# Kernel optimization log

Measured on AMD Instinct MI355X. Metric: run time of the kernel, lower is better.

Reference implementation:

```python
import jax, jax.numpy as jnp
import numpy as np

C = 256      # MSA_channels
PC = 256     # pair_channels
G = 4        # groups
GP = C // G  # group_planes
FF = 4 * C
EPS = 1e-5


def layernorm(x, w, b):
    mu = jnp.mean(x, axis=-1, keepdims=True)
    var = jnp.mean(jnp.square(x - mu), axis=-1, keepdims=True)
    return (x - mu) * jax.lax.rsqrt(var + EPS) * w + b


def setup_inputs() -> dict:
    key = jax.random.key(0)
    ks = jax.random.split(key, 12)
    N, D, L = 1, 64, 512
    s = lambda fan_in: 1.0 / np.sqrt(fan_in)
    return {
        "msa_matrix": jax.random.normal(ks[0], (N, D, L, C), jnp.float32),
        "rr_edge": jax.random.normal(ks[1], (N, L, L, PC), jnp.float32),
        "ln_msa_w": jnp.ones((C,), jnp.float32),
        "ln_msa_b": jnp.zeros((C,), jnp.float32),
        "ln_rr_w": jnp.ones((PC,), jnp.float32),
        "ln_rr_b": jnp.zeros((PC,), jnp.float32),
        "WA": jax.random.normal(ks[2], (PC, G), jnp.float32) * s(PC),
        "bA": jnp.zeros((G,), jnp.float32),
        "WV": jax.random.normal(ks[3], (C, C), jnp.float32) * s(C),
        "bV": jnp.zeros((C,), jnp.float32),
        "WO": jax.random.normal(ks[4], (C, C), jnp.float32) * s(C),
        "bO": jnp.zeros((C,), jnp.float32),
        "ln_ff_w": jnp.ones((C,), jnp.float32),
        "ln_ff_b": jnp.zeros((C,), jnp.float32),
        "W1": jax.random.normal(ks[5], (C, FF), jnp.float32) * s(C),
        "b1": jnp.zeros((FF,), jnp.float32),
        "W2": jax.random.normal(ks[6], (FF, C), jnp.float32) * s(FF),
        "b2": jnp.zeros((C,), jnp.float32),
    }


def reference(msa_matrix, rr_edge, ln_msa_w, ln_msa_b, ln_rr_w, ln_rr_b,
              WA, bA, WV, bV, WO, bO, ln_ff_w, ln_ff_b, W1, b1, W2, b2):
    N, D, L, _ = msa_matrix.shape
    raw = msa_matrix
    m = layernorm(msa_matrix, ln_msa_w, ln_msa_b)          # [N,D,L,C]
    E = 0.5 * (rr_edge + jnp.swapaxes(rr_edge, 1, 2))      # symmetrize [N,L,L,PC]
    E = layernorm(E, ln_rr_w, ln_rr_b)
    A = jax.nn.softmax(E @ WA + bA, axis=2)                # [N,L,L,G], softmax over key dim j
    V = (m @ WV + bV).reshape(N, D, L, G, GP)              # [N,D,L,G,GP]
    agg = jnp.einsum('nijg,ndjgc->ndigc', A, V).reshape(N, D, L, C)
    out = agg @ WO + bO
    x = raw + out                                          # residual (dropout = identity at eval)
    h = layernorm(x, ln_ff_w, ln_ff_b)                     # FFN with pre-LN + residual
    return x + (jax.nn.relu(h @ W1 + b1) @ W2 + b2)
```

## Files before the change

### kernel.cpp

```cpp
#include <hip/hip_runtime.h>
#include <hip/hip_bf16.h>

typedef __bf16 bf16;
typedef bf16 bf16x8 __attribute__((ext_vector_type(8)));
typedef bf16 bf16x4v __attribute__((ext_vector_type(4)));
typedef float f32x4 __attribute__((ext_vector_type(4)));

#define LN_EPS 1e-5f

__device__ __forceinline__ void gload_lds16(const bf16* gsrc, bf16* ldst) {
  __builtin_amdgcn_global_load_lds(
      (const __attribute__((address_space(1))) void*)gsrc,
      (__attribute__((address_space(3))) void*)ldst, 16, 0, 0);
}

__global__ __launch_bounds__(256) void ln_rows_kernel(
    const float* __restrict__ in, const float* __restrict__ w,
    const float* __restrict__ b, bf16* __restrict__ out)
{
  int row = blockIdx.x * 4 + (threadIdx.x >> 6);
  int lane = threadIdx.x & 63;
  const float4* p = (const float4*)(in + (size_t)row * 256);
  float4 v = p[lane];
  float s = v.x + v.y + v.z + v.w;
  float q = v.x*v.x + v.y*v.y + v.z*v.z + v.w*v.w;
  #pragma unroll
  for (int o = 32; o; o >>= 1) { s += __shfl_xor(s, o); q += __shfl_xor(q, o); }
  float mu = s * (1.0f/256.0f);
  float rs = rsqrtf(q*(1.0f/256.0f) - mu*mu + LN_EPS);
  float4 wv = ((const float4*)w)[lane];
  float4 bv = ((const float4*)b)[lane];
  bf16x4v o4;
  o4[0] = (bf16)((v.x - mu)*rs*wv.x + bv.x);
  o4[1] = (bf16)((v.y - mu)*rs*wv.y + bv.y);
  o4[2] = (bf16)((v.z - mu)*rs*wv.z + bv.z);
  o4[3] = (bf16)((v.w - mu)*rs*wv.w + bv.w);
  *(bf16x4v*)(out + (size_t)row * 256 + lane * 4) = o4;
}

__global__ __launch_bounds__(256) void transpose_all_kernel(
    const float* __restrict__ WV, const float* __restrict__ WO,
    const float* __restrict__ W1, const float* __restrict__ W2,
    bf16* __restrict__ WVt, bf16* __restrict__ WOt,
    bf16* __restrict__ W1t, bf16* __restrict__ W2t)
{
  __shared__ float tile[32][33];
  int id = blockIdx.x;
  const float* in; bf16* out; int R, C, tpr;
  if (id < 64)       { in = WV; out = WVt; R = 256;  C = 256;  tpr = 8;  }
  else if (id < 128) { in = WO; out = WOt; R = 256;  C = 256;  tpr = 8;  id -= 64; }
  else if (id < 384) { in = W1; out = W1t; R = 256;  C = 1024; tpr = 32; id -= 128; }
  else               { in = W2; out = W2t; R = 1024; C = 256;  tpr = 8;  id -= 384; }
  int bc = (id % tpr) * 32, br = (id / tpr) * 32;
  int tx = threadIdx.x, ty = threadIdx.y;
  #pragma unroll
  for (int i = ty; i < 32; i += 8)
    tile[i][tx] = in[(size_t)(br + i) * C + bc + tx];
  __syncthreads();
  #pragma unroll
  for (int i = ty; i < 32; i += 8)
    out[(size_t)(bc + i) * R + br + tx] = (bf16)tile[tx][i];
}

__global__ __launch_bounds__(256) void sym_ln_wa_kernel(
    const float* __restrict__ rr, const float* __restrict__ w,
    const float* __restrict__ b, const float* __restrict__ WA,
    float* __restrict__ S)
{
  int rem = blockIdx.x; int ti = 0; int len = 32;
  while (rem >= len) { rem -= len; ti++; len--; }
  int tj = ti + rem;
  int wid = threadIdx.x >> 6, lane = threadIdx.x & 63;
  int c0 = lane * 4;
  float4 wv = ((const float4*)w)[lane];
  float4 bv = ((const float4*)b)[lane];
  const float4* wa4 = (const float4*)WA;
  float4 wa0 = wa4[c0+0], wa1 = wa4[c0+1], wa2 = wa4[c0+2], wa3 = wa4[c0+3];
  int pend = blockIdx.y * 64 + 64;
  for (int p = blockIdx.y * 64 + wid; p < pend; p += 4) {
    int i = ti*16 + (p >> 4), j = tj*16 + (p & 15);
    float4 a = ((const float4*)(rr + ((size_t)i*512 + j)*256))[lane];
    float4 c = ((const float4*)(rr + ((size_t)j*512 + i)*256))[lane];
    float ex = 0.5f*(a.x + c.x), ey = 0.5f*(a.y + c.y),
          ez = 0.5f*(a.z + c.z), ew = 0.5f*(a.w + c.w);
    float s = ex+ey+ez+ew;
    float q = ex*ex+ey*ey+ez*ez+ew*ew;
    #pragma unroll
    for (int o = 32; o; o >>= 1) { s += __shfl_xor(s, o); q += __shfl_xor(q, o); }
    float mu = s*(1.f/256.f);
    float rs = rsqrtf(q*(1.f/256.f) - mu*mu + LN_EPS);
    float nx = (ex-mu)*rs*wv.x + bv.x;
    float ny = (ey-mu)*rs*wv.y + bv.y;
    float nz = (ez-mu)*rs*wv.z + bv.z;
    float nw = (ew-mu)*rs*wv.w + bv.w;
    float g0 = nx*wa0.x + ny*wa1.x + nz*wa2.x + nw*wa3.x;
    float g1 = nx*wa0.y + ny*wa1.y + nz*wa2.y + nw*wa3.y;
    float g2 = nx*wa0.z + ny*wa1.z + nz*wa2.z + nw*wa3.z;
    float g3 = nx*wa0.w + ny*wa1.w + nz*wa2.w + nw*wa3.w;
    #pragma unroll
    for (int o = 32; o; o >>= 1) {
      g0 += __shfl_xor(g0, o); g1 += __shfl_xor(g1, o);
      g2 += __shfl_xor(g2, o); g3 += __shfl_xor(g3, o);
    }
    if (lane == 0) {
      float4 r4 = make_float4(g0, g1, g2, g3);
      ((float4*)S)[(size_t)i*512 + j] = r4;
      ((float4*)S)[(size_t)j*512 + i] = r4;
    }
  }
}

__global__ __launch_bounds__(256) void softmax_kernel(
    const float* __restrict__ S, bf16* __restrict__ Aout)
{
  int i = blockIdx.x * 4 + (threadIdx.x >> 6);
  int lane = threadIdx.x & 63;
  const float4* Sr = (const float4*)S + (size_t)i * 512;
  float4 s[8];
  float m0 = -1e30f, m1 = -1e30f, m2 = -1e30f, m3 = -1e30f;
  #pragma unroll
  for (int it = 0; it < 8; it++) {
    s[it] = Sr[lane + it*64];
    m0 = fmaxf(m0, s[it].x); m1 = fmaxf(m1, s[it].y);
    m2 = fmaxf(m2, s[it].z); m3 = fmaxf(m3, s[it].w);
  }
  #pragma unroll
  for (int o = 32; o; o >>= 1) {
    m0 = fmaxf(m0, __shfl_xor(m0, o)); m1 = fmaxf(m1, __shfl_xor(m1, o));
    m2 = fmaxf(m2, __shfl_xor(m2, o)); m3 = fmaxf(m3, __shfl_xor(m3, o));
  }
  float t0=0.f, t1=0.f, t2=0.f, t3=0.f;
  #pragma unroll
  for (int it = 0; it < 8; it++) {
    s[it].x = __expf(s[it].x - m0); t0 += s[it].x;
    s[it].y = __expf(s[it].y - m1); t1 += s[it].y;
    s[it].z = __expf(s[it].z - m2); t2 += s[it].z;
    s[it].w = __expf(s[it].w - m3); t3 += s[it].w;
  }
  #pragma unroll
  for (int o = 32; o; o >>= 1) {
    t0 += __shfl_xor(t0, o); t1 += __shfl_xor(t1, o);
    t2 += __shfl_xor(t2, o); t3 += __shfl_xor(t3, o);
  }
  t0 = 1.f/t0; t1 = 1.f/t1; t2 = 1.f/t2; t3 = 1.f/t3;
  bf16* A0 = Aout + (size_t)i * 512;
  #pragma unroll
  for (int it = 0; it < 8; it++) {
    int j = lane + it*64;
    A0[j]          = (bf16)(s[it].x * t0);
    A0[262144 + j] = (bf16)(s[it].y * t1);
    A0[524288 + j] = (bf16)(s[it].z * t2);
    A0[786432 + j] = (bf16)(s[it].w * t3);
  }
}

template<int MODE>
__global__ __launch_bounds__(256) void gemm_bt_kernel(
    const bf16* __restrict__ Aglob, const bf16* __restrict__ Bglob,
    void* __restrict__ outP, const float* __restrict__ bias,
    const float* __restrict__ resid, int M, int N, int K)
{
  __shared__ bf16 As[128 * 32];
  __shared__ bf16 Bs[128 * 32];
  int g = blockIdx.z;
  const bf16* Ag = Aglob;
  const bf16* Bg = Bglob;
  if (MODE == 1) { Ag += (size_t)g * 512 * 512; Bg += (size_t)g * 4096 * 512; }
  int bm = blockIdx.y * 128, bn = blockIdx.x * 128;
  int tid = threadIdx.x;
  int wid = tid >> 6, lane = tid & 63;
  int wm = (wid >> 1) * 64, wn = (wid & 1) * 64;
  f32x4 acc[4][4];
  #pragma unroll
  for (int mi = 0; mi < 4; mi++)
    #pragma unroll
    for (int ni = 0; ni < 4; ni++)
      acc[mi][ni] = (f32x4){0.f, 0.f, 0.f, 0.f};
  int c0 = wid * 2, c1 = wid * 2 + 1;
  int srow = lane >> 2;
  int scol = (lane & 3) * 8;
  const bf16* a0 = &Ag[(size_t)(bm + c0*16 + srow) * K + scol];
  const bf16* a1 = &Ag[(size_t)(bm + c1*16 + srow) * K + scol];
  const bf16* b0 = &Bg[(size_t)(bn + c0*16 + srow) * K + scol];
  const bf16* b1 = &Bg[(size_t)(bn + c1*16 + srow) * K + scol];
  int fr = lane & 15, fk = (lane >> 4) * 8;
  for (int k0 = 0; k0 < K; k0 += 32) {
    __syncthreads();
    gload_lds16(a0 + k0, &As[c0 * 512]);
    gload_lds16(a1 + k0, &As[c1 * 512]);
    gload_lds16(b0 + k0, &Bs[c0 * 512]);
    gload_lds16(b1 + k0, &Bs[c1 * 512]);
    __syncthreads();
    bf16x8 af[4], bf_[4];
    #pragma unroll
    for (int mi = 0; mi < 4; mi++) af[mi] = *(const bf16x8*)&As[(wm + mi*16 + fr) * 32 + fk];
    #pragma unroll
    for (int ni = 0; ni < 4; ni++) bf_[ni] = *(const bf16x8*)&Bs[(wn + ni*16 + fr) * 32 + fk];
    #pragma unroll
    for (int mi = 0; mi < 4; mi++)
      #pragma unroll
      for (int ni = 0; ni < 4; ni++)
        acc[mi][ni] = __builtin_amdgcn_mfma_f32_16x16x32_bf16(af[mi], bf_[ni], acc[mi][ni], 0, 0, 0);
  }
  int cn0 = lane & 15;
  int rq = (lane >> 4) * 4;
  #pragma unroll
  for (int mi = 0; mi < 4; mi++) {
    #pragma unroll
    for (int ni = 0; ni < 4; ni++) {
      int mb = bm + wm + mi*16 + rq;
      int nc = bn + wn + ni*16 + cn0;
      #pragma unroll
      for (int r = 0; r < 4; r++) {
        int mr = mb + r;
        float v = acc[mi][ni][r];
        if (MODE == 0) {
          v += bias[mr];
          int gg = mr >> 6, rp = mr & 63, d = nc >> 9, j = nc & 511;
          ((bf16*)outP)[((size_t)gg*4096 + d*64 + rp)*512 + j] = (bf16)v;
        } else if (MODE == 1) {
          int d = nc >> 6, c6 = nc & 63;
          ((bf16*)outP)[((size_t)d*512 + mr)*256 + g*64 + c6] = (bf16)v;
        } else if (MODE == 2) {
          v += bias[nc] + resid[(size_t)mr * N + nc];
          ((float*)outP)[(size_t)mr * N + nc] = v;
        } else {
          v = fmaxf(v + bias[nc], 0.f);
          ((bf16*)outP)[(size_t)mr * N + nc] = (bf16)v;
        }
      }
    }
  }
}

extern "C" void kernel_launch(void* const* d_in, const int* in_sizes, int n_in,
                              void* d_out, int out_size, void* d_ws, size_t ws_size,
                              hipStream_t stream)
{
  (void)in_sizes; (void)n_in; (void)out_size; (void)ws_size;
  const float* msa = (const float*)d_in[0];
  const float* rr  = (const float*)d_in[1];
  const float* lmw = (const float*)d_in[2];
  const float* lmb = (const float*)d_in[3];
  const float* lrw = (const float*)d_in[4];
  const float* lrb = (const float*)d_in[5];
  const float* WA  = (const float*)d_in[6];
  const float* WV  = (const float*)d_in[8];
  const float* bV  = (const float*)d_in[9];
  const float* WO  = (const float*)d_in[10];
  const float* bO  = (const float*)d_in[11];
  const float* lfw = (const float*)d_in[12];
  const float* lfb = (const float*)d_in[13];
  const float* W1  = (const float*)d_in[14];
  const float* b1  = (const float*)d_in[15];
  const float* W2  = (const float*)d_in[16];
  const float* b2  = (const float*)d_in[17];
  float* out = (float*)d_out;
  char* ws = (char*)d_ws;
  bf16* tbuf = (bf16*)(ws + 0);
  float* S   = (float*)(ws + 0);
  bf16* Abuf = (bf16*)(ws + 4194304);
  bf16* m    = (bf16*)(ws + 6291456);
  bf16* Vt   = (bf16*)(ws + 23068672);
  bf16* agg  = (bf16*)(ws + 39845888);
  bf16* h    = (bf16*)(ws + 67108864);
  bf16* WVt  = (bf16*)(ws + 83886080);
  bf16* WOt  = WVt + 65536;
  bf16* W1t  = WOt + 65536;
  bf16* W2t  = W1t + 262144;

  transpose_all_kernel<<<640, dim3(32, 8), 0, stream>>>(WV, WO, W1, W2, WVt, WOt, W1t, W2t);

  ln_rows_kernel<<<8192, 256, 0, stream>>>(msa, lmw, lmb, m);
  sym_ln_wa_kernel<<<dim3(528, 4), 256, 0, stream>>>(rr, lrw, lrb, WA, S);
  gemm_bt_kernel<0><<<dim3(256, 2, 1), 256, 0, stream>>>(WVt, m, Vt, bV, nullptr, 256, 32768, 256);
  softmax_kernel<<<128, 256, 0, stream>>>(S, Abuf);
  gemm_bt_kernel<1><<<dim3(32, 4, 4), 256, 0, stream>>>(Abuf, Vt, agg, nullptr, nullptr, 512, 4096, 512);
  gemm_bt_kernel<2><<<dim3(2, 256, 1), 256, 0, stream>>>(agg, WOt, out, bO, msa, 32768, 256, 256);
  ln_rows_kernel<<<8192, 256, 0, stream>>>(out, lfw, lfb, h);
  gemm_bt_kernel<3><<<dim3(8, 256, 1), 256, 0, stream>>>(h, W1t, tbuf, b1, nullptr, 32768, 1024, 256);
  gemm_bt_kernel<2><<<dim3(2, 256, 1), 256, 0, stream>>>(tbuf, W2t, out, b2, out, 32768, 256, 1024);
}
```

Baseline: 249.6 us.

## Fuse FFN layernorm, W1 GEMM+ReLU, and W2 GEMM+residual into one kernel

Replaces the separate LN, W1 GEMM and W2 GEMM launches with a single kernel that processes 128 rows per block. It normalizes the rows into LDS, computes the 1024-wide hidden activation in 256-column chunks kept in LDS, and accumulates the W2 product in registers before adding the residual. This removes the global round trips for the h and hidden-activation buffers. The cost is only 256 blocks with about 136KB of LDS each, which means low occupancy. The per-chunk GEMM loops are also not pipelined and synchronize twice per k-step.

```diff
diff --git a/kernel.cpp b/kernel.cpp
--- a/kernel.cpp
+++ b/kernel.cpp
@@ -221,13 +221,154 @@
         } else if (MODE == 1) {
           int d = nc >> 6, c6 = nc & 63;
           ((bf16*)outP)[((size_t)d*512 + mr)*256 + g*64 + c6] = (bf16)v;
-        } else if (MODE == 2) {
+        } else {
           v += bias[nc] + resid[(size_t)mr * N + nc];
           ((float*)outP)[(size_t)mr * N + nc] = v;
-        } else {
-          v = fmaxf(v + bias[nc], 0.f);
-          ((bf16*)outP)[(size_t)mr * N + nc] = (bf16)v;
         }
+      }
+    }
+  }
+}
+
+__global__ __launch_bounds__(512, 2) void ffn_fused_kernel(
+    const float* __restrict__ x, const float* __restrict__ lnw,
+    const float* __restrict__ lnb, const bf16* __restrict__ W1t,
+    const float* __restrict__ b1, const bf16* __restrict__ W2t,
+    const float* __restrict__ b2, float* __restrict__ out)
+{
+  __shared__ __align__(16) char hbuf[128 * 512];
+  __shared__ __align__(16) char tbuf[128 * 512];
+  __shared__ __align__(16) bf16 Bs[256 * 32];
+  int tid = threadIdx.x;
+  int wid = tid >> 6, lane = tid & 63;
+  size_t row0 = (size_t)blockIdx.x * 128;
+
+  {
+    float4 wv = ((const float4*)lnw)[lane];
+    float4 bv = ((const float4*)lnb)[lane];
+    for (int it = 0; it < 16; it++) {
+      int row = wid * 16 + it;
+      float4 v = ((const float4*)(x + (row0 + row) * 256))[lane];
+      float s = v.x+v.y+v.z+v.w, q = v.x*v.x+v.y*v.y+v.z*v.z+v.w*v.w;
+      #pragma unroll
+      for (int o = 32; o; o >>= 1) { s += __shfl_xor(s, o); q += __shfl_xor(q, o); }
+      float mu = s * (1.f/256.f);
+      float rs = rsqrtf(q*(1.f/256.f) - mu*mu + LN_EPS);
+      bf16x4v o4;
+      o4[0] = (bf16)((v.x-mu)*rs*wv.x + bv.x);
+      o4[1] = (bf16)((v.y-mu)*rs*wv.y + bv.y);
+      o4[2] = (bf16)((v.z-mu)*rs*wv.z + bv.z);
+      o4[3] = (bf16)((v.w-mu)*rs*wv.w + bv.w);
+      *(bf16x4v*)(hbuf + row*512 + ((lane*8) ^ ((row & 7) << 4))) = o4;
+    }
+  }
+  __syncthreads();
+
+  int wm = (wid >> 2) * 64;
+  int wn = (wid & 3) * 64;
+  int fr = lane & 15;
+  int fk2 = ((lane >> 4) * 8) * 2;
+  int cn0 = lane & 15, rq = (lane >> 4) * 4;
+  int arow[4], asw[4], boff[4];
+  #pragma unroll
+  for (int mi = 0; mi < 4; mi++) {
+    arow[mi] = wm + mi*16 + fr;
+    asw[mi]  = (arow[mi] & 7) << 4;
+  }
+  #pragma unroll
+  for (int ni = 0; ni < 4; ni++) {
+    int br = wn + ni*16 + fr;
+    boff[ni] = br*64 + (fk2 ^ (((br >> 1) & 3) << 4));
+  }
+  int srow = tid >> 2;
+  int ps = tid & 3;
+
+  f32x4 acc2[4][4];
+  #pragma unroll
+  for (int mi = 0; mi < 4; mi++)
+    #pragma unroll
+    for (int ni = 0; ni < 4; ni++)
+      acc2[mi][ni] = (f32x4){0.f, 0.f, 0.f, 0.f};
+
+  for (int cf = 0; cf < 4; cf++) {
+    f32x4 acc1[4][4];
+    #pragma unroll
+    for (int mi = 0; mi < 4; mi++)
+      #pragma unroll
+      for (int ni = 0; ni < 4; ni++)
+        acc1[mi][ni] = (f32x4){0.f, 0.f, 0.f, 0.f};
+    for (int k0 = 0; k0 < 256; k0 += 32) {
+      __syncthreads();
+      #pragma unroll
+      for (int q = 0; q < 2; q++) {
+        int r = q*128 + srow;
+        int ls = ps ^ ((r >> 1) & 3);
+        gload_lds16(W1t + (size_t)(cf*256 + r) * 256 + k0 + ls*8,
+                    Bs + q*4096 + wid*512);
+      }
+      __syncthreads();
+      bf16x8 af[4], bf_[4];
+      #pragma unroll
+      for (int mi = 0; mi < 4; mi++)
+        af[mi] = *(const bf16x8*)(hbuf + arow[mi]*512 + ((k0*2 + fk2) ^ asw[mi]));
+      #pragma unroll
+      for (int ni = 0; ni < 4; ni++)
+        bf_[ni] = *(const bf16x8*)((const char*)Bs + boff[ni]);
+      #pragma unroll
+      for (int mi = 0; mi < 4; mi++)
+        #pragma unroll
+        for (int ni = 0; ni < 4; ni++)
+          acc1[mi][ni] = __builtin_amdgcn_mfma_f32_16x16x32_bf16(af[mi], bf_[ni], acc1[mi][ni], 0, 0, 0);
+    }
+    __syncthreads();
+    #pragma unroll
+    for (int ni = 0; ni < 4; ni++) {
+      int col = wn + ni*16 + cn0;
+      float bb = b1[cf*256 + col];
+      #pragma unroll
+      for (int mi = 0; mi < 4; mi++) {
+        #pragma unroll
+        for (int r = 0; r < 4; r++) {
+          int row = wm + mi*16 + rq + r;
+          float v = fmaxf(acc1[mi][ni][r] + bb, 0.f);
+          *(bf16*)(tbuf + row*512 + ((col*2) ^ ((row & 7) << 4))) = (bf16)v;
+        }
+      }
+    }
+    for (int k0 = 0; k0 < 256; k0 += 32) {
+      __syncthreads();
+      #pragma unroll
+      for (int q = 0; q < 2; q++) {
+        int r = q*128 + srow;
+        int ls = ps ^ ((r >> 1) & 3);
+        gload_lds16(W2t + (size_t)r * 1024 + cf*256 + k0 + ls*8,
+                    Bs + q*4096 + wid*512);
+      }
+      __syncthreads();
+      bf16x8 af[4], bf_[4];
+      #pragma unroll
+      for (int mi = 0; mi < 4; mi++)
+        af[mi] = *(const bf16x8*)(tbuf + arow[mi]*512 + ((k0*2 + fk2) ^ asw[mi]));
+      #pragma unroll
+      for (int ni = 0; ni < 4; ni++)
+        bf_[ni] = *(const bf16x8*)((const char*)Bs + boff[ni]);
+      #pragma unroll
+      for (int mi = 0; mi < 4; mi++)
+        #pragma unroll
+        for (int ni = 0; ni < 4; ni++)
+          acc2[mi][ni] = __builtin_amdgcn_mfma_f32_16x16x32_bf16(af[mi], bf_[ni], acc2[mi][ni], 0, 0, 0);
+    }
+  }
+  #pragma unroll
+  for (int ni = 0; ni < 4; ni++) {
+    int col = wn + ni*16 + cn0;
+    float bb = b2[col];
+    #pragma unroll
+    for (int mi = 0; mi < 4; mi++) {
+      #pragma unroll
+      for (int r = 0; r < 4; r++) {
+        size_t grow = row0 + wm + mi*16 + rq + r;
+        out[grow*256 + col] = x[grow*256 + col] + acc2[mi][ni][r] + bb;
       }
     }
   }
@@ -257,13 +398,11 @@
   const float* b2  = (const float*)d_in[17];
   float* out = (float*)d_out;
   char* ws = (char*)d_ws;
-  bf16* tbuf = (bf16*)(ws + 0);
   float* S   = (float*)(ws + 0);
   bf16* Abuf = (bf16*)(ws + 4194304);
   bf16* m    = (bf16*)(ws + 6291456);
   bf16* Vt   = (bf16*)(ws + 23068672);
   bf16* agg  = (bf16*)(ws + 39845888);
-  bf16* h    = (bf16*)(ws + 67108864);
   bf16* WVt  = (bf16*)(ws + 83886080);
   bf16* WOt  = WVt + 65536;
   bf16* W1t  = WOt + 65536;
@@ -277,7 +416,5 @@
   softmax_kernel<<<128, 256, 0, stream>>>(S, Abuf);
   gemm_bt_kernel<1><<<dim3(32, 4, 4), 256, 0, stream>>>(Abuf, Vt, agg, nullptr, nullptr, 512, 4096, 512);
   gemm_bt_kernel<2><<<dim3(2, 256, 1), 256, 0, stream>>>(agg, WOt, out, bO, msa, 32768, 256, 256);
-  ln_rows_kernel<<<8192, 256, 0, stream>>>(out, lfw, lfb, h);
-  gemm_bt_kernel<3><<<dim3(8, 256, 1), 256, 0, stream>>>(h, W1t, tbuf, b1, nullptr, 32768, 1024, 256);
-  gemm_bt_kernel<2><<<dim3(2, 256, 1), 256, 0, stream>>>(tbuf, W2t, out, b2, out, 32768, 256, 1024);
-}
+  ffn_fused_kernel<<<256, 512, 0, stream>>>(out, lfw, lfb, W1t, b1, W2t, b2, out);
+}
```

Measured after the change: 242.9 us. 1.03x faster.

## Triple-buffer LDS tiles in GEMM with async prefetch two steps ahead

Applied to the files above, without the earlier changes.

Replaces the single-buffered LDS load/compute loop in the bf16 MFMA GEMM with a three-stage ring buffer. Direct global-to-LDS loads are issued two K-tiles ahead, and explicit vmcnt waits plus barriers gate each compute step. The goal is to hide global memory latency behind MFMA work instead of stalling on every tile. In exchange the GEMM uses three times the LDS, which may lower occupancy, and correctness now depends on the hand-tuned waitcnt counts.

```diff
diff --git a/kernel.cpp b/kernel.cpp
--- a/kernel.cpp
+++ b/kernel.cpp
@@ -160,8 +160,8 @@
     void* __restrict__ outP, const float* __restrict__ bias,
     const float* __restrict__ resid, int M, int N, int K)
 {
-  __shared__ bf16 As[128 * 32];
-  __shared__ bf16 Bs[128 * 32];
+  __shared__ bf16 As[3][128 * 32];
+  __shared__ bf16 Bs[3][128 * 32];
   int g = blockIdx.z;
   const bf16* Ag = Aglob;
   const bf16* Bg = Bglob;
@@ -184,23 +184,47 @@
   const bf16* b0 = &Bg[(size_t)(bn + c0*16 + srow) * K + scol];
   const bf16* b1 = &Bg[(size_t)(bn + c1*16 + srow) * K + scol];
   int fr = lane & 15, fk = (lane >> 4) * 8;
-  for (int k0 = 0; k0 < K; k0 += 32) {
-    __syncthreads();
-    gload_lds16(a0 + k0, &As[c0 * 512]);
-    gload_lds16(a1 + k0, &As[c1 * 512]);
-    gload_lds16(b0 + k0, &Bs[c0 * 512]);
-    gload_lds16(b1 + k0, &Bs[c1 * 512]);
-    __syncthreads();
+  int nt = K >> 5;
+  gload_lds16(a0, &As[0][c0 * 512]);
+  gload_lds16(a1, &As[0][c1 * 512]);
+  gload_lds16(b0, &Bs[0][c0 * 512]);
+  gload_lds16(b1, &Bs[0][c1 * 512]);
+  if (nt > 1) {
+    gload_lds16(a0 + 32, &As[1][c0 * 512]);
+    gload_lds16(a1 + 32, &As[1][c1 * 512]);
+    gload_lds16(b0 + 32, &Bs[1][c0 * 512]);
+    gload_lds16(b1 + 32, &Bs[1][c1 * 512]);
+  }
+  int cur = 0, pf = 2;
+  for (int t = 0; t < nt; t++) {
+    if (t + 2 < nt) {
+      int k2 = (t + 2) << 5;
+      gload_lds16(a0 + k2, &As[pf][c0 * 512]);
+      gload_lds16(a1 + k2, &As[pf][c1 * 512]);
+      gload_lds16(b0 + k2, &Bs[pf][c0 * 512]);
+      gload_lds16(b1 + k2, &Bs[pf][c1 * 512]);
+      asm volatile("s_waitcnt vmcnt(8)" ::: "memory");
+    } else if (t + 1 < nt) {
+      asm volatile("s_waitcnt vmcnt(4)" ::: "memory");
+    } else {
+      asm volatile("s_waitcnt vmcnt(0)" ::: "memory");
+    }
+    __builtin_amdgcn_s_barrier();
+    __builtin_amdgcn_sched_barrier(0);
     bf16x8 af[4], bf_[4];
     #pragma unroll
-    for (int mi = 0; mi < 4; mi++) af[mi] = *(const bf16x8*)&As[(wm + mi*16 + fr) * 32 + fk];
-    #pragma unroll
-    for (int ni = 0; ni < 4; ni++) bf_[ni] = *(const bf16x8*)&Bs[(wn + ni*16 + fr) * 32 + fk];
+    for (int mi = 0; mi < 4; mi++) af[mi] = *(const bf16x8*)&As[cur][(wm + mi*16 + fr) * 32 + fk];
+    #pragma unroll
+    for (int ni = 0; ni < 4; ni++) bf_[ni] = *(const bf16x8*)&Bs[cur][(wn + ni*16 + fr) * 32 + fk];
     #pragma unroll
     for (int mi = 0; mi < 4; mi++)
       #pragma unroll
       for (int ni = 0; ni < 4; ni++)
         acc[mi][ni] = __builtin_amdgcn_mfma_f32_16x16x32_bf16(af[mi], bf_[ni], acc[mi][ni], 0, 0, 0);
+    __builtin_amdgcn_sched_barrier(0);
+    __builtin_amdgcn_s_barrier();
+    cur = (cur == 2) ? 0 : cur + 1;
+    pf  = (pf == 2)  ? 0 : pf + 1;
   }
   int cn0 = lane & 15;
   int rq = (lane >> 4) * 4;
```

New measurement: 246.2 us. About the same (-1.4%).
